# Optimization experiments

Hardware: AMD Instinct MI355X
Metric: run time of the kernel (lower is better)

The kernel has to match this reference:

```python
import jax, jax.numpy as jnp
import numpy as np

GROUPS = 32
EPS = 1e-6


def group_norm(x, gamma, beta):
    # x: [B, C, T], normalize per group of channels over (C//G, T)
    B, C, T = x.shape
    xr = x.reshape(B, GROUPS, C // GROUPS, T)
    mean = xr.mean(axis=(2, 3), keepdims=True)
    var = xr.var(axis=(2, 3), keepdims=True)
    xn = ((xr - mean) * jax.lax.rsqrt(var + EPS)).reshape(B, C, T)
    return xn * gamma[None, :, None] + beta[None, :, None]


def conv1x1(h, w, b):
    # 1x1 Conv1d == channel matmul. h: [B,C,T], w: [O,C], b: [O]
    return jnp.einsum('oc,bct->bot', w, h) + b[None, :, None]


def setup_inputs() -> dict:
    key = jax.random.key(0)
    ks = jax.random.split(key, 10)
    B, C, T = 8, 512, 2048
    s = 1.0 / np.sqrt(C)
    return {
        'x': jax.random.normal(ks[0], (B, C, T), jnp.float32),
        'gamma': jnp.ones((C,), jnp.float32),
        'beta': jnp.zeros((C,), jnp.float32),
        'q_w': jax.random.normal(ks[1], (C, C), jnp.float32) * s,
        'q_b': jnp.zeros((C,), jnp.float32),
        'k_w': jax.random.normal(ks[2], (C, C), jnp.float32) * s,
        'k_b': jnp.zeros((C,), jnp.float32),
        'v_w': jax.random.normal(ks[3], (C, C), jnp.float32) * s,
        'v_b': jnp.zeros((C,), jnp.float32),
        'o_w': jax.random.normal(ks[4], (C, C), jnp.float32) * s,
        'o_b': jnp.zeros((C,), jnp.float32),
    }


def reference(x, gamma, beta, q_w, q_b, k_w, k_b, v_w, v_b, o_w, o_b):
    h = group_norm(x, gamma, beta)
    q = conv1x1(h, q_w, q_b)  # [B,C,T]
    k = conv1x1(h, k_w, k_b)
    v = conv1x1(h, v_w, v_b)
    B, C, T = q.shape
    scale = jnp.asarray(C, q.dtype) ** -0.5
    # scores[b,t,s] = sum_c q[b,c,t] * k[b,c,s]
    scores = jnp.einsum('bct,bcs->bts', q, k) * scale
    w = jax.nn.softmax(scores, axis=-1)
    # out[b,c,t] = sum_s v[b,c,s] * w[b,t,s]
    h = jnp.einsum('bcs,bts->bct', v, w)
    h = conv1x1(h, o_w, o_b)
    return x + h
```

## Files before the change

### kernel.cpp

```cpp
#include <hip/hip_runtime.h>
#include <hip/hip_bf16.h>
#include <stdint.h>

typedef __bf16 bf16_t;
typedef __attribute__((ext_vector_type(8))) __bf16 bf16x8;
typedef __attribute__((ext_vector_type(4))) float f32x4;

__device__ __forceinline__ bool is_fp32(const void* gamma) {
  return ((const unsigned*)gamma)[0] == 0x3F800000u;
}

__device__ __forceinline__ void async_copy16(const bf16_t* g, bf16_t* l) {
  __builtin_amdgcn_global_load_lds(
      (const __attribute__((address_space(1))) void*)g,
      (__attribute__((address_space(3))) void*)l, 16, 0, 0);
}

__global__ __launch_bounds__(256) void prepass(
    const void* __restrict__ q_w, const void* __restrict__ k_w,
    const void* __restrict__ v_w, const void* __restrict__ o_w,
    const void* __restrict__ gamma, const void* __restrict__ beta,
    const void* __restrict__ q_b, const void* __restrict__ k_b,
    const void* __restrict__ v_b, const void* __restrict__ o_b,
    const void* __restrict__ xv, bf16_t* __restrict__ wdst,
    bf16_t* __restrict__ vdst, float* __restrict__ rowsum,
    float* __restrict__ stats) {
  const bool fp32 = is_fp32(gamma);
  int bid = blockIdx.x;
  int tid = threadIdx.x;
  if (bid < 4172) {
    int i = bid * 256 + tid;
    if (i < 1048576) {
      const void* wsrc[4] = {q_w, k_w, v_w, o_w};
      int seg = i >> 18, off = i & 262143;
      const void* s = wsrc[seg];
      wdst[i] = fp32 ? (bf16_t)((const float*)s)[off] : ((const bf16_t*)s)[off];
    } else {
      int j = i - 1048576;
      if (j < 3072) {
        const void* vsrc[6] = {gamma, beta, q_b, k_b, v_b, o_b};
        int seg = j >> 9, off = j & 511;
        const void* s = vsrc[seg];
        vdst[j] =
            fp32 ? (bf16_t)((const float*)s)[off] : ((const bf16_t*)s)[off];
      } else {
        int j2 = j - 3072;
        if (j2 < 16384) rowsum[j2] = 0.0f;
      }
    }
    return;
  }
  int gidx = bid - 4172;
  long long base = (long long)gidx * 16 * 2048;
  float s = 0.f, q = 0.f;
#pragma unroll
  for (int ch = 0; ch < 16; ++ch) {
    long long off = base + (long long)ch * 2048 + tid * 8;
    float f[8];
    if (fp32) {
      const float* xf = (const float*)xv;
      float4 u = *(const float4*)(xf + off);
      float4 w = *(const float4*)(xf + off + 4);
      f[0] = u.x; f[1] = u.y; f[2] = u.z; f[3] = u.w;
      f[4] = w.x; f[5] = w.y; f[6] = w.z; f[7] = w.w;
    } else {
      bf16x8 vv = *(const bf16x8*)((const bf16_t*)xv + off);
#pragma unroll
      for (int e = 0; e < 8; ++e) f[e] = (float)vv[e];
    }
#pragma unroll
    for (int e = 0; e < 8; ++e) {
      s += f[e];
      q += f[e] * f[e];
    }
  }
  for (int o = 32; o > 0; o >>= 1) {
    s += __shfl_down(s, o);
    q += __shfl_down(q, o);
  }
  __shared__ float red[8];
  int wave = tid >> 6, lane = tid & 63;
  if (lane == 0) {
    red[wave] = s;
    red[4 + wave] = q;
  }
  __syncthreads();
  if (tid == 0) {
    stats[gidx * 2 + 0] = red[0] + red[1] + red[2] + red[3];
    stats[gidx * 2 + 1] = red[4] + red[5] + red[6] + red[7];
  }
}

__global__ __launch_bounds__(256) void gn_apply(const void* __restrict__ xv,
                                                const float* __restrict__ stats,
                                                const bf16_t* __restrict__ gammab,
                                                const bf16_t* __restrict__ betab,
                                                bf16_t* __restrict__ ht,
                                                const void* __restrict__ gamma) {
  const int C = 512, T = 2048;
  const bool fp32 = is_fp32(gamma);
  int bid = blockIdx.x;
  int ts = bid & 3;
  int gp = (bid >> 2) & 15;
  int b = bid >> 6;
  int tid = threadIdx.x;
  int c0 = gp * 32;
  int t0 = ts * 512;
  int cw = tid & 31;
  int gloc = cw >> 4;
  int gidx = b * 32 + gp * 2 + gloc;
  const float inv = 1.0f / 32768.0f;
  float mean = stats[gidx * 2] * inv;
  float var = stats[gidx * 2 + 1] * inv - mean * mean;
  float rstd = rsqrtf(var + 1e-6f);
  float sc = rstd * (float)gammab[c0 + cw];
  float sh = (float)betab[c0 + cw] - mean * sc;

  __shared__ bf16_t tile[32 * 68];
  const float* xf = (const float*)xv;
  const bf16_t* xb = (const bf16_t*)xv;
  long long xbase = ((long long)b * C + c0) * T + t0;
  bf16_t* hb = ht + ((long long)b * T + t0) * C + c0;
  for (int ch = 0; ch < 8; ++ch) {
#pragma unroll
    for (int s2 = 0; s2 < 8; ++s2) {
      int e = s2 * 256 + tid;
      int c = e >> 6, t = e & 63;
      long long off = xbase + (long long)c * T + ch * 64 + t;
      tile[c * 68 + t] = fp32 ? (bf16_t)xf[off] : xb[off];
    }
    __syncthreads();
#pragma unroll
    for (int s2 = 0; s2 < 8; ++s2) {
      int t = s2 * 8 + (tid >> 5);
      float v = (float)tile[cw * 68 + t];
      hb[(long long)(ch * 64 + t) * C + cw] = (bf16_t)(v * sc + sh);
    }
    __syncthreads();
  }
}

template <bool BIASM, bool BIASN, bool RESOUT, bool EXPSUM, bool NORMROW,
          int M, int N, int K, int LDA, int LDB, int LDC>
__device__ __forceinline__ void gemm_body(
    const bf16_t* __restrict__ A, long long sA, const bf16_t* __restrict__ B,
    long long sB, void* __restrict__ Cout, long long sC,
    const bf16_t* __restrict__ biasM, const bf16_t* __restrict__ biasN,
    const void* __restrict__ Res, long long sR, float alpha,
    const void* __restrict__ gamma, float* __restrict__ rowsum, int m0, int n0,
    int b, bf16_t* As, bf16_t* Bs) {
  const int tid = threadIdx.x;
  const int wave = tid >> 6;
  const int lane = tid & 63;
  const int lane15 = lane & 15;
  const int quad = lane >> 4;
  const bf16_t* Ab = A + (long long)b * sA + (long long)m0 * LDA;
  const bf16_t* Bb = B + (long long)b * sB + (long long)n0 * LDB;

  const int prow = wave * 32 + (lane >> 3);
  const int pcol = ((lane & 7) ^ (lane >> 3)) * 8;
  const int ldst = wave * 2048 + lane * 8;
  const int wm = (wave >> 1) << 6;
  const int wn = (wave & 1) << 6;
  const int swz = lane15 & 7;

  f32x4 acc[4][4] = {};

  for (int k0 = 0; k0 < K; k0 += 64) {
#pragma unroll
    for (int n = 0; n < 4; ++n) {
      async_copy16(Ab + (long long)(prow + n * 8) * LDA + k0 + pcol,
                   As + ldst + n * 512);
      async_copy16(Bb + (long long)(prow + n * 8) * LDB + k0 + pcol,
                   Bs + ldst + n * 512);
    }
    __syncthreads();
#pragma unroll
    for (int ks = 0; ks < 2; ++ks) {
      const int coff = (((ks << 2) + quad) ^ swz) * 8;
      bf16x8 af[4], bfr[4];
#pragma unroll
      for (int i = 0; i < 4; ++i)
        af[i] = *(const bf16x8*)&As[(wm + i * 16 + lane15) * 64 + coff];
#pragma unroll
      for (int j = 0; j < 4; ++j)
        bfr[j] = *(const bf16x8*)&Bs[(wn + j * 16 + lane15) * 64 + coff];
#pragma unroll
      for (int i = 0; i < 4; ++i)
#pragma unroll
        for (int j = 0; j < 4; ++j)
          acc[i][j] = __builtin_amdgcn_mfma_f32_16x16x32_bf16(
              af[i], bfr[j], acc[i][j], 0, 0, 0);
    }
    __syncthreads();
  }

  if (EXPSUM) {
#pragma unroll
    for (int i = 0; i < 4; ++i) {
#pragma unroll
      for (int r = 0; r < 4; ++r) {
        long long m = m0 + wm + i * 16 + quad * 4 + r;
        float partial = 0.f;
#pragma unroll
        for (int j = 0; j < 4; ++j) {
          long long n = n0 + wn + j * 16 + lane15;
          float v = __expf(acc[i][j][r] * alpha);
          partial += v;
          ((bf16_t*)Cout)[(long long)b * sC + m * LDC + n] = (bf16_t)v;
        }
        partial += __shfl_xor(partial, 1);
        partial += __shfl_xor(partial, 2);
        partial += __shfl_xor(partial, 4);
        partial += __shfl_xor(partial, 8);
        if (lane15 == 0) atomicAdd(&rowsum[(long long)b * M + m], partial);
      }
    }
    return;
  }

  float invr[4][4];
  if (NORMROW) {
#pragma unroll
    for (int i = 0; i < 4; ++i)
#pragma unroll
      for (int r = 0; r < 4; ++r)
        invr[i][r] =
            1.0f / rowsum[(long long)b * M + m0 + wm + i * 16 + quad * 4 + r];
  }
  bool fp32 = false;
  if (RESOUT) fp32 = is_fp32(gamma);
#pragma unroll
  for (int i = 0; i < 4; ++i) {
#pragma unroll
    for (int j = 0; j < 4; ++j) {
#pragma unroll
      for (int r = 0; r < 4; ++r) {
        long long m = m0 + wm + i * 16 + quad * 4 + r;
        long long n = n0 + wn + j * 16 + lane15;
        float v = acc[i][j][r] * alpha;
        if (NORMROW) v *= invr[i][r];
        if (BIASM) v += (float)biasM[m];
        if (BIASN) v += (float)biasN[n];
        long long idx = (long long)b * sC + m * LDC + n;
        if (RESOUT) {
          long long ridx = (long long)b * sR + m * LDC + n;
          if (fp32) {
            v += ((const float*)Res)[ridx];
            ((float*)Cout)[idx] = v;
          } else {
            v += (float)((const bf16_t*)Res)[ridx];
            ((bf16_t*)Cout)[idx] = (bf16_t)v;
          }
        } else {
          ((bf16_t*)Cout)[idx] = (bf16_t)v;
        }
      }
    }
  }
}

__global__ __launch_bounds__(256) void qkv_fat(
    const bf16_t* __restrict__ ht, const bf16_t* __restrict__ wqk,
    const bf16_t* __restrict__ wv, bf16_t* __restrict__ qkt,
    bf16_t* __restrict__ vvb, const bf16_t* __restrict__ qkb,
    const bf16_t* __restrict__ vbb, const void* __restrict__ gamma) {
  __shared__ __align__(16) bf16_t As[128 * 64];
  __shared__ __align__(16) bf16_t Bs[128 * 64];
  const long long TC = 2048LL * 512, CT = 512LL * 2048;
  int bid = blockIdx.x;
  if (bid < 1024) {
    int b = bid >> 7, rem = bid & 127;
    int n0 = (rem & 7) * 128, m0 = (rem >> 3) * 128;
    gemm_body<false, true, false, false, false, 2048, 1024, 512, 512, 512,
              1024>(ht, TC, wqk, 0, qkt, 2048LL * 1024, nullptr, qkb, nullptr,
                    0, 1.0f, gamma, nullptr, m0, n0, b, As, Bs);
  } else {
    int id2 = bid - 1024;
    int b = id2 >> 6, rem = id2 & 63;
    int n0 = (rem & 15) * 128, m0 = (rem >> 4) * 128;
    gemm_body<true, false, false, false, false, 512, 2048, 512, 512, 512,
              2048>(wv, 0, ht, TC, vvb, CT, vbb, nullptr, nullptr, 0, 1.0f,
                    gamma, nullptr, m0, n0, b, As, Bs);
  }
}

__global__ __launch_bounds__(256) void scores_kernel(
    const bf16_t* __restrict__ qkt, bf16_t* __restrict__ Sm,
    const void* __restrict__ gamma, float* __restrict__ rowsum, float alpha) {
  __shared__ __align__(16) bf16_t As[128 * 64];
  __shared__ __align__(16) bf16_t Bs[128 * 64];
  int fx = blockIdx.x;
  int gid = fx >> 4, win = fx & 15;
  int gm = gid & 3, gn = gid >> 2;
  int m0 = (gm * 4 + (win & 3)) * 128;
  int n0 = (gn * 4 + (win >> 2)) * 128;
  gemm_body<false, false, false, true, false, 2048, 2048, 512, 1024, 1024,
            2048>(qkt, 2048LL * 1024, qkt + 512, 2048LL * 1024, Sm,
                  2048LL * 2048, nullptr, nullptr, nullptr, 0, alpha, gamma,
                  rowsum, m0, n0, blockIdx.z, As, Bs);
}

__global__ __launch_bounds__(256) void av_kernel(const bf16_t* __restrict__ Sm,
                                                 const bf16_t* __restrict__ vvb,
                                                 bf16_t* __restrict__ h2t,
                                                 const void* __restrict__ gamma,
                                                 float* __restrict__ rowsum) {
  __shared__ __align__(16) bf16_t As[128 * 64];
  __shared__ __align__(16) bf16_t Bs[128 * 64];
  gemm_body<false, false, false, false, true, 2048, 512, 2048, 2048, 2048,
            512>(Sm, 2048LL * 2048, vvb, 512LL * 2048, h2t, 2048LL * 512,
                 nullptr, nullptr, nullptr, 0, 1.0f, gamma, rowsum,
                 blockIdx.y * 128, blockIdx.x * 128, blockIdx.z, As, Bs);
}

__global__ __launch_bounds__(256) void final_kernel(
    const bf16_t* __restrict__ wo, const bf16_t* __restrict__ h2t,
    void* __restrict__ out, const bf16_t* __restrict__ obb,
    const void* __restrict__ x, const void* __restrict__ gamma) {
  __shared__ __align__(16) bf16_t As[128 * 64];
  __shared__ __align__(16) bf16_t Bs[128 * 64];
  const long long TC = 2048LL * 512, CT = 512LL * 2048;
  gemm_body<true, false, true, false, false, 512, 2048, 512, 512, 512, 2048>(
      wo, 0, h2t, TC, out, CT, obb, nullptr, x, CT, 1.0f, gamma, nullptr,
      blockIdx.y * 128, blockIdx.x * 128, blockIdx.z, As, Bs);
}

extern "C" void kernel_launch(void* const* d_in, const int* in_sizes, int n_in,
                              void* d_out, int out_size, void* d_ws,
                              size_t ws_size, hipStream_t stream) {
  const void* x = d_in[0];
  const void* gamma = d_in[1];
  const void* beta = d_in[2];
  const void* q_w = d_in[3];
  const void* q_b = d_in[4];
  const void* k_w = d_in[5];
  const void* k_b = d_in[6];
  const void* v_w = d_in[7];
  const void* v_b = d_in[8];
  const void* o_w = d_in[9];
  const void* o_b = d_in[10];

  const long long BTC = 8LL * 2048 * 512;
  char* ws = (char*)d_ws;
  float* stats = (float*)(ws + 256);
  bf16_t* wq = (bf16_t*)(ws + 4096);
  bf16_t* wv = wq + 2 * 262144;
  bf16_t* wo = wq + 3 * 262144;
  bf16_t* vdst = wq + 4 * 262144;
  bf16_t* gammab = vdst + 0 * 512;
  bf16_t* betab = vdst + 1 * 512;
  bf16_t* qkb = vdst + 2 * 512;
  bf16_t* vbb = vdst + 4 * 512;
  bf16_t* obb = vdst + 5 * 512;
  float* rowsum = (float*)(ws + 4096 + 2 * 1024 * 1024 + 8192);
  const size_t hdr = 4096 + 2 * 1024 * 1024 + 8192 + 65536;
  bf16_t* ht = (bf16_t*)(ws + hdr);
  bf16_t* vvb = ht + BTC;
  bf16_t* Sm = vvb + BTC;
  bf16_t* h2t = ht;
  bf16_t* qkt = (bf16_t*)d_out;

  const float scale = 0.044194173824159216f;

  prepass<<<4428, 256, 0, stream>>>(q_w, k_w, v_w, o_w, gamma, beta, q_b, k_b,
                                    v_b, o_b, x, wq, vdst, rowsum, stats);
  gn_apply<<<512, 256, 0, stream>>>(x, stats, gammab, betab, ht, gamma);
  qkv_fat<<<1536, 256, 0, stream>>>(ht, wq, wv, qkt, vvb, qkb, vbb, gamma);
  scores_kernel<<<dim3(256, 1, 8), 256, 0, stream>>>(qkt, Sm, gamma, rowsum,
                                                     scale);
  av_kernel<<<dim3(4, 16, 8), 256, 0, stream>>>(Sm, vvb, h2t, gamma, rowsum);
  final_kernel<<<dim3(16, 4, 8), 256, 0, stream>>>(wo, h2t, d_out, obb, x,
                                                   gamma);
}
```

Baseline: 292.2 us.

## Replace GEMM core with 256x256-tile, 8-wave, 4-stage pipelined LDS schedule

Every GEMM stage now uses a new body with 256x256 output tiles computed by 512 threads (8 waves). K is split into 32-wide slabs held in a four-region LDS ring of 128 KB, and global-to-LDS async copies are interleaved with MFMA phases behind explicit barriers, waitcnts and setprio. The goal is more data reuse per tile and overlap of loads with compute in place of the old load-sync-compute loop. In exchange each block holds 128 accumulator fp32x4 per lane and far fewer blocks are launched (e.g. 128 for av/final), which risks register pressure and poor CU fill on the MI355X.

```diff
diff --git a/kernel.cpp b/kernel.cpp
--- a/kernel.cpp
+++ b/kernel.cpp
@@ -14,6 +14,16 @@
   __builtin_amdgcn_global_load_lds(
       (const __attribute__((address_space(1))) void*)g,
       (__attribute__((address_space(3))) void*)l, 16, 0, 0);
+}
+
+#define GFENCE() asm volatile("" ::: "memory")
+
+__device__ __forceinline__ void hard_barrier() {
+  GFENCE();
+  __builtin_amdgcn_sched_barrier(0);
+  __builtin_amdgcn_s_barrier();
+  __builtin_amdgcn_sched_barrier(0);
+  GFENCE();
 }
 
 __global__ __launch_bounds__(256) void prepass(
@@ -142,69 +152,133 @@
 
 template <bool BIASM, bool BIASN, bool RESOUT, bool EXPSUM, bool NORMROW,
           int M, int N, int K, int LDA, int LDB, int LDC>
-__device__ __forceinline__ void gemm_body(
+__device__ __forceinline__ void gemm8_body(
     const bf16_t* __restrict__ A, long long sA, const bf16_t* __restrict__ B,
     long long sB, void* __restrict__ Cout, long long sC,
     const bf16_t* __restrict__ biasM, const bf16_t* __restrict__ biasN,
     const void* __restrict__ Res, long long sR, float alpha,
     const void* __restrict__ gamma, float* __restrict__ rowsum, int m0, int n0,
-    int b, bf16_t* As, bf16_t* Bs) {
+    int b, bf16_t* lds) {
   const int tid = threadIdx.x;
-  const int wave = tid >> 6;
   const int lane = tid & 63;
   const int lane15 = lane & 15;
   const int quad = lane >> 4;
+  const int wave = tid >> 6;
+  const int wm = wave >> 2;
+  const int wn = wave & 3;
+
   const bf16_t* Ab = A + (long long)b * sA + (long long)m0 * LDA;
   const bf16_t* Bb = B + (long long)b * sB + (long long)n0 * LDB;
 
-  const int prow = wave * 32 + (lane >> 3);
-  const int pcol = ((lane & 7) ^ (lane >> 3)) * 8;
-  const int ldst = wave * 2048 + lane * 8;
-  const int wm = (wave >> 1) << 6;
-  const int wn = (wave & 1) << 6;
-  const int swz = lane15 & 7;
-
-  f32x4 acc[4][4] = {};
-
-  for (int k0 = 0; k0 < K; k0 += 64) {
-#pragma unroll
-    for (int n = 0; n < 4; ++n) {
-      async_copy16(Ab + (long long)(prow + n * 8) * LDA + k0 + pcol,
-                   As + ldst + n * 512);
-      async_copy16(Bb + (long long)(prow + n * 8) * LDB + k0 + pcol,
-                   Bs + ldst + n * 512);
-    }
-    __syncthreads();
-#pragma unroll
-    for (int ks = 0; ks < 2; ++ks) {
-      const int coff = (((ks << 2) + quad) ^ swz) * 8;
-      bf16x8 af[4], bfr[4];
-#pragma unroll
-      for (int i = 0; i < 4; ++i)
-        af[i] = *(const bf16x8*)&As[(wm + i * 16 + lane15) * 64 + coff];
-#pragma unroll
-      for (int j = 0; j < 4; ++j)
-        bfr[j] = *(const bf16x8*)&Bs[(wn + j * 16 + lane15) * 64 + coff];
-#pragma unroll
-      for (int i = 0; i < 4; ++i)
-#pragma unroll
-        for (int j = 0; j < 4; ++j)
-          acc[i][j] = __builtin_amdgcn_mfma_f32_16x16x32_bf16(
-              af[i], bfr[j], acc[i][j], 0, 0, 0);
-    }
-    __syncthreads();
-  }
+  const int R00 = 0, R01 = 8192, R10 = 16384, R11 = 24576;
+  bf16_t* ldsA = lds;
+  bf16_t* ldsB = lds + 32768;
+
+  const int srow = tid >> 2;
+  const int sg = ((tid & 3) - (srow >> 1)) & 3;
+  const bf16_t* As_src = Ab + (long long)srow * LDA + sg * 8;
+  const bf16_t* Bs_src = Bb + (long long)srow * LDB + sg * 8;
+  const long long A128 = 128LL * LDA, B128 = 128LL * LDB;
+  bf16_t* ldsAw = ldsA + tid * 8;
+  bf16_t* ldsBw = ldsB + tid * 8;
+
+  auto stA = [&](int kelem, int reg) {
+    async_copy16(As_src + kelem, ldsAw + reg);
+    async_copy16(As_src + A128 + kelem, ldsAw + reg + 4096);
+  };
+  auto stB = [&](int kelem, int reg) {
+    async_copy16(Bs_src + kelem, ldsBw + reg);
+    async_copy16(Bs_src + B128 + kelem, ldsBw + reg + 4096);
+  };
+
+  const int slot = ((quad + (lane15 >> 1)) & 3) * 8;
+  const int aoff = (wm * 128 + lane15) * 32 + slot;
+  const int boff = (wn * 64 + lane15) * 32 + slot;
+
+  bf16x8 af[8];
+  f32x4 acc[8][4] = {};
+
+  auto lda_frags = [&](int reg) {
+#pragma unroll
+    for (int i = 0; i < 8; ++i)
+      af[i] = *(const bf16x8*)(ldsA + reg + aoff + i * 512);
+  };
+  auto ldbf = [&](int reg, int j) {
+    return *(const bf16x8*)(ldsB + reg + boff + j * 512);
+  };
+
+  auto phaseA = [&](int rdA, int rdB, int stk, int streg) {
+    lda_frags(rdA);
+    bf16x8 b0 = ldbf(rdB, 0), b1 = ldbf(rdB, 1);
+    stA(stk, streg);
+    hard_barrier();
+    asm volatile("s_waitcnt lgkmcnt(0)" ::: "memory");
+    __builtin_amdgcn_sched_barrier(0);
+    __builtin_amdgcn_s_setprio(1);
+#pragma unroll
+    for (int i = 0; i < 8; ++i) {
+      acc[i][0] = __builtin_amdgcn_mfma_f32_16x16x32_bf16(af[i], b0, acc[i][0], 0, 0, 0);
+      acc[i][1] = __builtin_amdgcn_mfma_f32_16x16x32_bf16(af[i], b1, acc[i][1], 0, 0, 0);
+    }
+    __builtin_amdgcn_s_setprio(0);
+    hard_barrier();
+  };
+  auto phaseB = [&](int rdB, int stk, int streg) {
+    bf16x8 b0 = ldbf(rdB, 2), b1 = ldbf(rdB, 3);
+    stB(stk, streg);
+    hard_barrier();
+    asm volatile("s_waitcnt lgkmcnt(0)" ::: "memory");
+    __builtin_amdgcn_sched_barrier(0);
+    __builtin_amdgcn_s_setprio(1);
+#pragma unroll
+    for (int i = 0; i < 8; ++i) {
+      acc[i][2] = __builtin_amdgcn_mfma_f32_16x16x32_bf16(af[i], b0, acc[i][2], 0, 0, 0);
+      acc[i][3] = __builtin_amdgcn_mfma_f32_16x16x32_bf16(af[i], b1, acc[i][3], 0, 0, 0);
+    }
+    __builtin_amdgcn_s_setprio(0);
+    asm volatile("s_waitcnt vmcnt(8)" ::: "memory");
+    hard_barrier();
+  };
+
+  const int NT = K / 64;
+  const int NI = NT / 2;
+
+  stA(0, R00);
+  stB(0, R00);
+  stA(32, R01);
+  stB(32, R01);
+  stA(64, R10);
+  stB(64, R10);
+  asm volatile("s_waitcnt vmcnt(8)" ::: "memory");
+  hard_barrier();
+
+#pragma unroll 1
+  for (int it = 0; it < NI; ++it) {
+    const int ku = it * 128;
+    const bool last = (it == NI - 1);
+    const int ku2 = last ? 0 : ku + 128;
+    const int kv2 = last ? 64 : ku + 192;
+    phaseA(R00, R00, ku + 96, R11);
+    phaseB(R00, ku + 96, R11);
+    phaseA(R01, R01, ku2, R00);
+    phaseB(R01, ku2, R00);
+    phaseA(R10, R10, ku2 + 32, R01);
+    phaseB(R10, ku2 + 32, R01);
+    phaseA(R11, R11, kv2, R10);
+    phaseB(R11, kv2, R10);
+  }
+  asm volatile("s_waitcnt vmcnt(0)" ::: "memory");
 
   if (EXPSUM) {
 #pragma unroll
-    for (int i = 0; i < 4; ++i) {
+    for (int i = 0; i < 8; ++i) {
 #pragma unroll
       for (int r = 0; r < 4; ++r) {
-        long long m = m0 + wm + i * 16 + quad * 4 + r;
+        long long m = m0 + wm * 128 + i * 16 + quad * 4 + r;
         float partial = 0.f;
 #pragma unroll
         for (int j = 0; j < 4; ++j) {
-          long long n = n0 + wn + j * 16 + lane15;
+          long long n = n0 + wn * 64 + j * 16 + lane15;
           float v = __expf(acc[i][j][r] * alpha);
           partial += v;
           ((bf16_t*)Cout)[(long long)b * sC + m * LDC + n] = (bf16_t)v;
@@ -219,25 +293,25 @@
     return;
   }
 
-  float invr[4][4];
+  float invr[8][4];
   if (NORMROW) {
 #pragma unroll
-    for (int i = 0; i < 4; ++i)
+    for (int i = 0; i < 8; ++i)
 #pragma unroll
       for (int r = 0; r < 4; ++r)
-        invr[i][r] =
-            1.0f / rowsum[(long long)b * M + m0 + wm + i * 16 + quad * 4 + r];
+        invr[i][r] = 1.0f / rowsum[(long long)b * M + m0 + wm * 128 + i * 16 +
+                                   quad * 4 + r];
   }
   bool fp32 = false;
   if (RESOUT) fp32 = is_fp32(gamma);
 #pragma unroll
-  for (int i = 0; i < 4; ++i) {
+  for (int i = 0; i < 8; ++i) {
 #pragma unroll
     for (int j = 0; j < 4; ++j) {
 #pragma unroll
       for (int r = 0; r < 4; ++r) {
-        long long m = m0 + wm + i * 16 + quad * 4 + r;
-        long long n = n0 + wn + j * 16 + lane15;
+        long long m = m0 + wm * 128 + i * 16 + quad * 4 + r;
+        long long n = n0 + wn * 64 + j * 16 + lane15;
         float v = acc[i][j][r] * alpha;
         if (NORMROW) v *= invr[i][r];
         if (BIASM) v += (float)biasM[m];
@@ -260,70 +334,65 @@
   }
 }
 
-__global__ __launch_bounds__(256) void qkv_fat(
+__global__ __launch_bounds__(512, 2) void qkv_fat(
     const bf16_t* __restrict__ ht, const bf16_t* __restrict__ wqk,
     const bf16_t* __restrict__ wv, bf16_t* __restrict__ qkt,
     bf16_t* __restrict__ vvb, const bf16_t* __restrict__ qkb,
     const bf16_t* __restrict__ vbb, const void* __restrict__ gamma) {
-  __shared__ __align__(16) bf16_t As[128 * 64];
-  __shared__ __align__(16) bf16_t Bs[128 * 64];
+  __shared__ __align__(16) bf16_t lds[65536];
   const long long TC = 2048LL * 512, CT = 512LL * 2048;
   int bid = blockIdx.x;
-  if (bid < 1024) {
-    int b = bid >> 7, rem = bid & 127;
-    int n0 = (rem & 7) * 128, m0 = (rem >> 3) * 128;
-    gemm_body<false, true, false, false, false, 2048, 1024, 512, 512, 512,
-              1024>(ht, TC, wqk, 0, qkt, 2048LL * 1024, nullptr, qkb, nullptr,
-                    0, 1.0f, gamma, nullptr, m0, n0, b, As, Bs);
+  if (bid < 256) {
+    int b = bid >> 5, rem = bid & 31;
+    int n0 = (rem & 3) * 256, m0 = (rem >> 2) * 256;
+    gemm8_body<false, true, false, false, false, 2048, 1024, 512, 512, 512,
+               1024>(ht, TC, wqk, 0, qkt, 2048LL * 1024, nullptr, qkb, nullptr,
+                     0, 1.0f, gamma, nullptr, m0, n0, b, lds);
   } else {
-    int id2 = bid - 1024;
-    int b = id2 >> 6, rem = id2 & 63;
-    int n0 = (rem & 15) * 128, m0 = (rem >> 4) * 128;
-    gemm_body<true, false, false, false, false, 512, 2048, 512, 512, 512,
-              2048>(wv, 0, ht, TC, vvb, CT, vbb, nullptr, nullptr, 0, 1.0f,
-                    gamma, nullptr, m0, n0, b, As, Bs);
-  }
-}
-
-__global__ __launch_bounds__(256) void scores_kernel(
+    int id2 = bid - 256;
+    int b = id2 >> 4, rem = id2 & 15;
+    int m0 = (rem & 1) * 256, n0 = (rem >> 1) * 256;
+    gemm8_body<true, false, false, false, false, 512, 2048, 512, 512, 512,
+               2048>(wv, 0, ht, TC, vvb, CT, vbb, nullptr, nullptr, 0, 1.0f,
+                     gamma, nullptr, m0, n0, b, lds);
+  }
+}
+
+__global__ __launch_bounds__(512, 2) void scores_kernel(
     const bf16_t* __restrict__ qkt, bf16_t* __restrict__ Sm,
     const void* __restrict__ gamma, float* __restrict__ rowsum, float alpha) {
-  __shared__ __align__(16) bf16_t As[128 * 64];
-  __shared__ __align__(16) bf16_t Bs[128 * 64];
-  int fx = blockIdx.x;
-  int gid = fx >> 4, win = fx & 15;
-  int gm = gid & 3, gn = gid >> 2;
-  int m0 = (gm * 4 + (win & 3)) * 128;
-  int n0 = (gn * 4 + (win >> 2)) * 128;
-  gemm_body<false, false, false, true, false, 2048, 2048, 512, 1024, 1024,
-            2048>(qkt, 2048LL * 1024, qkt + 512, 2048LL * 1024, Sm,
-                  2048LL * 2048, nullptr, nullptr, nullptr, 0, alpha, gamma,
-                  rowsum, m0, n0, blockIdx.z, As, Bs);
-}
-
-__global__ __launch_bounds__(256) void av_kernel(const bf16_t* __restrict__ Sm,
-                                                 const bf16_t* __restrict__ vvb,
-                                                 bf16_t* __restrict__ h2t,
-                                                 const void* __restrict__ gamma,
-                                                 float* __restrict__ rowsum) {
-  __shared__ __align__(16) bf16_t As[128 * 64];
-  __shared__ __align__(16) bf16_t Bs[128 * 64];
-  gemm_body<false, false, false, false, true, 2048, 512, 2048, 2048, 2048,
-            512>(Sm, 2048LL * 2048, vvb, 512LL * 2048, h2t, 2048LL * 512,
-                 nullptr, nullptr, nullptr, 0, 1.0f, gamma, rowsum,
-                 blockIdx.y * 128, blockIdx.x * 128, blockIdx.z, As, Bs);
-}
-
-__global__ __launch_bounds__(256) void final_kernel(
+  __shared__ __align__(16) bf16_t lds[65536];
+  int x = blockIdx.x;
+  int gid = x >> 4, win = x & 15;
+  int gm = gid & 1, gn = gid >> 1;
+  int m0 = (gm * 4 + (win & 3)) * 256;
+  int n0 = (gn * 4 + (win >> 2)) * 256;
+  gemm8_body<false, false, false, true, false, 2048, 2048, 512, 1024, 1024,
+             2048>(qkt, 2048LL * 1024, qkt + 512, 2048LL * 1024, Sm,
+                   2048LL * 2048, nullptr, nullptr, nullptr, 0, alpha, gamma,
+                   rowsum, m0, n0, blockIdx.z, lds);
+}
+
+__global__ __launch_bounds__(512, 2) void av_kernel(
+    const bf16_t* __restrict__ Sm, const bf16_t* __restrict__ vvb,
+    bf16_t* __restrict__ h2t, const void* __restrict__ gamma,
+    float* __restrict__ rowsum) {
+  __shared__ __align__(16) bf16_t lds[65536];
+  gemm8_body<false, false, false, false, true, 2048, 512, 2048, 2048, 2048,
+             512>(Sm, 2048LL * 2048, vvb, 512LL * 2048, h2t, 2048LL * 512,
+                  nullptr, nullptr, nullptr, 0, 1.0f, gamma, rowsum,
+                  blockIdx.y * 256, blockIdx.x * 256, blockIdx.z, lds);
+}
+
+__global__ __launch_bounds__(512, 2) void final_kernel(
     const bf16_t* __restrict__ wo, const bf16_t* __restrict__ h2t,
     void* __restrict__ out, const bf16_t* __restrict__ obb,
     const void* __restrict__ x, const void* __restrict__ gamma) {
-  __shared__ __align__(16) bf16_t As[128 * 64];
-  __shared__ __align__(16) bf16_t Bs[128 * 64];
+  __shared__ __align__(16) bf16_t lds[65536];
   const long long TC = 2048LL * 512, CT = 512LL * 2048;
-  gemm_body<true, false, true, false, false, 512, 2048, 512, 512, 512, 2048>(
+  gemm8_body<true, false, true, false, false, 512, 2048, 512, 512, 512, 2048>(
       wo, 0, h2t, TC, out, CT, obb, nullptr, x, CT, 1.0f, gamma, nullptr,
-      blockIdx.y * 128, blockIdx.x * 128, blockIdx.z, As, Bs);
+      blockIdx.y * 256, blockIdx.x * 256, blockIdx.z, lds);
 }
 
 extern "C" void kernel_launch(void* const* d_in, const int* in_sizes, int n_in,
@@ -366,10 +435,10 @@
   prepass<<<4428, 256, 0, stream>>>(q_w, k_w, v_w, o_w, gamma, beta, q_b, k_b,
                                     v_b, o_b, x, wq, vdst, rowsum, stats);
   gn_apply<<<512, 256, 0, stream>>>(x, stats, gammab, betab, ht, gamma);
-  qkv_fat<<<1536, 256, 0, stream>>>(ht, wq, wv, qkt, vvb, qkb, vbb, gamma);
-  scores_kernel<<<dim3(256, 1, 8), 256, 0, stream>>>(qkt, Sm, gamma, rowsum,
-                                                     scale);
-  av_kernel<<<dim3(4, 16, 8), 256, 0, stream>>>(Sm, vvb, h2t, gamma, rowsum);
-  final_kernel<<<dim3(16, 4, 8), 256, 0, stream>>>(wo, h2t, d_out, obb, x,
-                                                   gamma);
-}
+  qkv_fat<<<384, 512, 0, stream>>>(ht, wq, wv, qkt, vvb, qkb, vbb, gamma);
+  scores_kernel<<<dim3(64, 1, 8), 512, 0, stream>>>(qkt, Sm, gamma, rowsum,
+                                                    scale);
+  av_kernel<<<dim3(2, 8, 8), 512, 0, stream>>>(Sm, vvb, h2t, gamma, rowsum);
+  final_kernel<<<dim3(8, 2, 8), 512, 0, stream>>>(wo, h2t, d_out, obb, x,
+                                                  gamma);
+}
```

Result: slower. 330.9 us (+13.2%).
